# Kernel optimization log

Hardware: AMD Instinct MI355X
Metric: run time of the kernel (lower is better)

Reference implementation:

```python
import jax, jax.numpy as jnp
import numpy as np

B, J, C = 8, 2048, 256
K = 32
H = 8
D = 32  # out_dim per head


def setup_inputs() -> dict:
    key = jax.random.key(0)
    k0, k1, k2, k3, k4, k5 = jax.random.split(key, 6)
    x = jax.random.normal(k0, (B, J, C), dtype=jnp.float32)
    nbr_idx = jax.random.randint(k1, (B, J, K), 0, J)
    s_in = 1.0 / np.sqrt(C)
    s_hd = 1.0 / np.sqrt(H * D)
    Wq = jax.random.uniform(k2, (C, H * D), dtype=jnp.float32, minval=-s_in, maxval=s_in)
    Wk = jax.random.uniform(k3, (C, H * D), dtype=jnp.float32, minval=-s_in, maxval=s_in)
    Wv = jax.random.uniform(k4, (C, H * D), dtype=jnp.float32, minval=-s_in, maxval=s_in)
    Wp = jax.random.uniform(k5, (H * D, D), dtype=jnp.float32, minval=-s_hd, maxval=s_hd)
    return {"x": x, "nbr_idx": nbr_idx, "Wq": Wq, "Wk": Wk, "Wv": Wv, "Wp": Wp}


def reference(x, nbr_idx, Wq, Wk, Wv, Wp):
    b, j, c = x.shape
    q = (x @ Wq).reshape(b, j, H, D)  # [B,J,H,D]
    k = (x @ Wk).reshape(b, j, H, D)
    v = (x @ Wv).reshape(b, j, H, D)
    bidx = jnp.arange(b)[:, None, None]  # [B,1,1]
    k_nbr = k[bidx, nbr_idx]  # [B,J,K,H,D]
    v_nbr = v[bidx, nbr_idx]  # [B,J,K,H,D]
    attn = jnp.einsum("bjhd,bjkhd->bjkh", q, k_nbr) / np.sqrt(D)
    attn = jax.nn.leaky_relu(attn, negative_slope=0.2)
    attn = jax.nn.softmax(attn, axis=2)  # softmax over K neighbors
    out = jnp.einsum("bjkh,bjkhd->bjhd", attn, v_nbr).reshape(b, j, H * D)
    return out @ Wp  # [B,J,D]
```

## Files before the change

### kernel.cpp

```cpp
#include <hip/hip_runtime.h>
#include <hip/hip_bf16.h>


typedef short bf16x8 __attribute__((ext_vector_type(8)));
typedef float f32x4  __attribute__((ext_vector_type(4)));
typedef float f32x2  __attribute__((ext_vector_type(2)));
typedef _Float16 h16x2 __attribute__((ext_vector_type(2)));

__device__ __forceinline__ float bf2f(unsigned short u) {
    union { unsigned int i; float f; } c; c.i = ((unsigned int)u) << 16; return c.f;
}
__device__ __forceinline__ unsigned short f2bf(float f) {
    union { float f; unsigned int i; } c; c.f = f;
    unsigned int r = c.i + 0x7FFFu + ((c.i >> 16) & 1u);
    return (unsigned short)(r >> 16);
}
__device__ __forceinline__ unsigned short f2h(float f) {
    union { _Float16 h; unsigned short u; } c; c.h = (_Float16)f;
    return c.u;
}
__device__ __forceinline__ f32x2 upk(unsigned int u) {
    union { unsigned int i; float f; } lo, hi;
    lo.i = u << 16;
    hi.i = u & 0xffff0000u;
    return (f32x2){lo.f, hi.f};
}

#if defined(__has_builtin)
#if __has_builtin(__builtin_amdgcn_fdot2)
#define HAVE_FDOT2 1
#endif
#endif
__device__ __forceinline__ float dot2acc(unsigned int a, unsigned int b, float acc) {
#ifdef HAVE_FDOT2
    union { unsigned int u; h16x2 v; } ca, cb;
    ca.u = a; cb.u = b;
    return __builtin_amdgcn_fdot2(ca.v, cb.v, acc, false);
#else
    union { unsigned int u; _Float16 h[2]; } ca, cb;
    ca.u = a; cb.u = b;
    return acc + (float)ca.h[0] * (float)cb.h[0] + (float)ca.h[1] * (float)cb.h[1];
#endif
}

__device__ __forceinline__ void gld_lds16(void* lds, const void* g) {
    __builtin_amdgcn_global_load_lds(
        (const __attribute__((address_space(1))) unsigned int*)g,
        (__attribute__((address_space(3))) unsigned int*)lds,
        16, 0, 0);
}

__global__ __launch_bounds__(256) void prep(
    const float* __restrict__ x,
    const float* __restrict__ Wq, const float* __restrict__ Wk,
    const float* __restrict__ Wv, const float* __restrict__ Wp,
    unsigned short* __restrict__ xb, unsigned short* __restrict__ Wt)
{
    const int blk = blockIdx.x, tid = threadIdx.x;
    if (blk < 4096) {
        int t = blk * 256 + tid;
        float4 f = ((const float4*)x)[t];
        ushort4 u;
        u.x = f2bf(f.x); u.y = f2bf(f.y); u.z = f2bf(f.z); u.w = f2bf(f.w);
        ((ushort4*)xb)[t] = u;
        return;
    }
    int wi = blk - 4096;
    int w = wi >> 8, n = wi & 255, t = tid;
    if (w == 0) {
        Wt[(size_t)n * 256 + t] = f2bf(Wq[(size_t)t * 256 + n]);
    } else if (w == 1) {
        Wt[(size_t)(256 + n) * 256 + t] = f2bf(Wk[(size_t)t * 256 + n]);
    } else {
        int h = n >> 5, c = n & 31;
        float acc = 0.f;
#pragma unroll
        for (int d = 0; d < 32; d++)
            acc += Wv[(size_t)t * 256 + h * 32 + d] * Wp[(size_t)(h * 32 + d) * 32 + c];
        Wt[(size_t)(512 + n) * 256 + t] = f2bf(acc);
    }
}

__global__ __launch_bounds__(256) void qkv_mfma(
    const unsigned short* __restrict__ xb,
    const unsigned short* __restrict__ Wt,
    unsigned short* __restrict__ Q, unsigned short* __restrict__ Kp,
    unsigned short* __restrict__ VP)
{
    __shared__ unsigned short Als[128][64];
    __shared__ unsigned short Bls[128][64];

    const unsigned short* Wb = Wt + (size_t)blockIdx.z * 65536;
    unsigned short* Y = (blockIdx.z == 0) ? Q : (blockIdx.z == 1) ? Kp : VP;
    const bool as_f16 = (blockIdx.z != 2);

    const int row0 = blockIdx.x * 128;
    const int col0 = blockIdx.y * 128;
    const int tid  = threadIdx.x;
    const int w    = tid >> 6, l = tid & 63;
    const int wm   = (w >> 1) * 64, wn = (w & 1) * 64;
    const int lm   = l & 15, quad = l >> 4;

    f32x4 acc[4][4];
#pragma unroll
    for (int i = 0; i < 4; i++)
#pragma unroll
        for (int j = 0; j < 4; j++) acc[i][j] = (f32x4){0.f, 0.f, 0.f, 0.f};

    const char* Ab = (const char*)(xb + (size_t)row0 * 256);
    const char* Bb = (const char*)(Wb + (size_t)col0 * 256);

    for (int k0 = 0; k0 < 256; k0 += 64) {
#pragma unroll
        for (int i = 0; i < 4; i++) {
            int s = i * 256 + tid;
            int r = s >> 3, c = s & 7;
            size_t go = (size_t)r * 512 + (size_t)k0 * 2 + c * 16;
            gld_lds16((char*)Als + s * 16, Ab + go);
            gld_lds16((char*)Bls + s * 16, Bb + go);
        }
        __syncthreads();

#pragma unroll
        for (int kk = 0; kk < 64; kk += 32) {
            bf16x8 a[4], b[4];
#pragma unroll
            for (int tm = 0; tm < 4; tm++)
                a[tm] = *(const bf16x8*)&Als[wm + tm * 16 + lm][kk + quad * 8];
#pragma unroll
            for (int tn = 0; tn < 4; tn++)
                b[tn] = *(const bf16x8*)&Bls[wn + tn * 16 + lm][kk + quad * 8];
#pragma unroll
            for (int tm = 0; tm < 4; tm++)
#pragma unroll
                for (int tn = 0; tn < 4; tn++)
                    acc[tm][tn] = __builtin_amdgcn_mfma_f32_16x16x32_bf16(
                        a[tm], b[tn], acc[tm][tn], 0, 0, 0);
        }
        __syncthreads();
    }

#pragma unroll
    for (int tm = 0; tm < 4; tm++) {
        int rbase = row0 + wm + tm * 16 + quad * 4;
#pragma unroll
        for (int tn = 0; tn < 4; tn++) {
            int col = col0 + wn + tn * 16 + lm;
            if (as_f16) {
#pragma unroll
                for (int r = 0; r < 4; r++)
                    Y[(size_t)(rbase + r) * 256 + col] = f2h(acc[tm][tn][r]);
            } else {
#pragma unroll
                for (int r = 0; r < 4; r++)
                    Y[(size_t)(rbase + r) * 256 + col] = f2bf(acc[tm][tn][r]);
            }
        }
    }
}

__global__ __launch_bounds__(256) void attn_wave(
    const unsigned short* __restrict__ qb,
    const unsigned short* __restrict__ kb,
    const unsigned short* __restrict__ vp,
    const int*            __restrict__ nbr,
    float*                __restrict__ out)
{
    const int beta = blockIdx.x;
    const int b    = beta & 7;
    const int jt   = beta >> 3;
    const int tid  = threadIdx.x;
    const int w    = tid >> 6;
    const int l    = tid & 63;
    const int lh   = l & 31;
    const int h5   = l >> 5;
    const int bj   = (b << 11) + jt * 4 + w;
    const size_t bbase = (size_t)b << 19;
    const int* nrow = nbr + (size_t)bj * 32;

    int ko = nrow[lh] << 8;
    int koff[16];
#pragma unroll
    for (int r = 0; r < 16; r++) koff[r] = __shfl(ko, 2 * r + h5);

    uint4 qu = *(const uint4*)(qb + (size_t)bj * 256 + lh * 8);

    uint4 kr[16];
#pragma unroll
    for (int r = 0; r < 16; r++)
        kr[r] = *(const uint4*)(kb + bbase + koff[r] + lh * 8);

    float s[16];
#pragma unroll
    for (int r = 0; r < 16; r++) {
        float a = 0.f;
        a = dot2acc(kr[r].x, qu.x, a);
        a = dot2acc(kr[r].y, qu.y, a);
        a = dot2acc(kr[r].z, qu.z, a);
        a = dot2acc(kr[r].w, qu.w, a);
        a += __shfl_xor(a, 1);
        a += __shfl_xor(a, 2);
        a *= 0.17677669529663687f;
        s[r] = (a > 0.f) ? a : 0.2f * a;
    }

    uint4 vr[16];
#pragma unroll
    for (int r = 0; r < 16; r++)
        vr[r] = *(const uint4*)(vp + bbase + koff[r] + lh * 8);

    float m = s[0];
#pragma unroll
    for (int r = 1; r < 16; r++) m = fmaxf(m, s[r]);
    m = fmaxf(m, __shfl_xor(m, 32));
    float sum = 0.f;
#pragma unroll
    for (int r = 0; r < 16; r++) { s[r] = __expf(s[r] - m); sum += s[r]; }
    sum += __shfl_xor(sum, 32);
    const float inv = 1.0f / sum;
#pragma unroll
    for (int r = 0; r < 16; r++) s[r] *= inv;

    f32x2 a0 = (f32x2){0.f, 0.f}, a1 = a0, a2 = a0, a3 = a0;
#pragma unroll
    for (int r = 0; r < 16; r++) {
        const f32x2 w2 = (f32x2){s[r], s[r]};
        a0 += upk(vr[r].x) * w2;
        a1 += upk(vr[r].y) * w2;
        a2 += upk(vr[r].z) * w2;
        a3 += upk(vr[r].w) * w2;
    }

    float o[8] = {a0.x, a0.y, a1.x, a1.y, a2.x, a2.y, a3.x, a3.y};
#pragma unroll
    for (int i = 0; i < 8; i++) o[i] += __shfl_xor(o[i], 32);
#pragma unroll
    for (int i = 0; i < 8; i++) o[i] += __shfl_xor(o[i], 4);
#pragma unroll
    for (int i = 0; i < 8; i++) o[i] += __shfl_xor(o[i], 8);
#pragma unroll
    for (int i = 0; i < 8; i++) o[i] += __shfl_xor(o[i], 16);

    if (l < 4) {
        float* op = out + (size_t)bj * 32 + l * 8;
        *(float4*)(op)     = make_float4(o[0], o[1], o[2], o[3]);
        *(float4*)(op + 4) = make_float4(o[4], o[5], o[6], o[7]);
    }
}

__global__ __launch_bounds__(256) void fused_all(
    const float* __restrict__ X, const int* __restrict__ nbr,
    const float* __restrict__ Wq, const float* __restrict__ Wk,
    const float* __restrict__ Wv, const float* __restrict__ Wp,
    float* __restrict__ out)
{
    __shared__ float xr[256], qrow[256], xn[256];
    __shared__ float vn[32][256];
    __shared__ int   nb[32];
    __shared__ float sc[32][8], pwv[32][8];
    __shared__ float sp[256], hd[256];
    __shared__ float red[8][32];

    const int bj = blockIdx.x, b = bj >> 11, tid = threadIdx.x;

    xr[tid] = X[(size_t)bj * 256 + tid];
    if (tid < 32) nb[tid] = nbr[(size_t)bj * 32 + tid];
    __syncthreads();

    {
        float acc = 0.f;
#pragma unroll 8
        for (int c = 0; c < 256; c++) acc += xr[c] * Wq[(size_t)c * 256 + tid];
        qrow[tid] = acc;
    }
    __syncthreads();

    for (int i = 0; i < 32; i++) {
        size_t r = (size_t)(b * 2048 + nb[i]);
        xn[tid] = X[r * 256 + tid];
        __syncthreads();
        float ka = 0.f, va = 0.f;
#pragma unroll 8
        for (int c = 0; c < 256; c++) {
            float xc = xn[c];
            ka += xc * Wk[(size_t)c * 256 + tid];
            va += xc * Wv[(size_t)c * 256 + tid];
        }
        vn[i][tid] = va;
        sp[tid] = qrow[tid] * ka;
        __syncthreads();
        if (tid < 8) {
            float s = 0.f;
#pragma unroll
            for (int d = 0; d < 32; d++) s += sp[tid * 32 + d];
            s *= 0.17677669529663687f;
            s = (s > 0.f) ? s : 0.2f * s;
            sc[i][tid] = s;
        }
        __syncthreads();
    }

    {
        const int h = tid & 7, kk = tid >> 3;
        float mx = -1e30f;
#pragma unroll
        for (int i = 0; i < 32; i++) mx = fmaxf(mx, sc[i][h]);
        float ssum = 0.f;
#pragma unroll
        for (int i = 0; i < 32; i++) ssum += __expf(sc[i][h] - mx);
        pwv[kk][h] = __expf(sc[kk][h] - mx) / ssum;
    }
    __syncthreads();

    {
        const int h2 = tid >> 5;
        float acc = 0.f;
#pragma unroll 8
        for (int i = 0; i < 32; i++) acc += pwv[i][h2] * vn[i][tid];
        hd[tid] = acc;
    }
    __syncthreads();

    {
        const int c = tid & 31, ch = tid >> 5;
        float p = 0.f;
#pragma unroll
        for (int i = 0; i < 32; i++) { int r = ch * 32 + i; p += hd[r] * Wp[r * 32 + c]; }
        red[ch][c] = p;
    }
    __syncthreads();

    if (tid < 32) {
        float o = 0.f;
#pragma unroll
        for (int i = 0; i < 8; i++) o += red[i][tid];
        out[(size_t)bj * 32 + tid] = o;
    }
}

extern "C" void kernel_launch(void* const* d_in, const int* in_sizes, int n_in,
                              void* d_out, int out_size, void* d_ws, size_t ws_size,
                              hipStream_t stream) {
    const float* x   = (const float*)d_in[0];
    const int*   nbr = (const int*)d_in[1];
    const float* Wq  = (const float*)d_in[2];
    const float* Wk  = (const float*)d_in[3];
    const float* Wv  = (const float*)d_in[4];
    const float* Wp  = (const float*)d_in[5];
    float*       out = (float*)d_out;

    const size_t ME   = (size_t)16384 * 256;
    const size_t need = (4 * ME + 3 * 65536) * sizeof(unsigned short);

    if (ws_size >= need) {
        unsigned short* q  = (unsigned short*)d_ws;
        unsigned short* k  = q + ME;
        unsigned short* vp = k + ME;
        unsigned short* xb = vp + ME;
        unsigned short* Wt = xb + ME;

        prep<<<4096 + 768, 256, 0, stream>>>(x, Wq, Wk, Wv, Wp, xb, Wt);
        qkv_mfma<<<dim3(128, 2, 3), 256, 0, stream>>>(xb, Wt, q, k, vp);
        attn_wave<<<4096, 256, 0, stream>>>(q, k, vp, nbr, out);
    } else {
        fused_all<<<16384, 256, 0, stream>>>(x, nbr, Wq, Wk, Wv, Wp, out);
    }
}
```

Before: 119.3 us.

## Double-buffer QKV GEMM LDS tiles with XOR swizzle and remapped 1D grid

Restructures the QKV projection GEMM to use a double-buffered LDS pipeline over 32-wide K steps. The next tile's global-to-LDS load is issued while MFMAs run on the current one. It adds an XOR swizzle on the 16-byte chunk index to reduce LDS bank conflicts. It also replaces the 3D grid with a 1D grid remapped so that consecutive blocks spread across XCDs while sharing row tiles. The cost is one barrier per K step instead of two per 64-wide step, plus extra index arithmetic; the overall GEMM is a modest share of the total runtime.

```diff
diff --git a/kernel.cpp b/kernel.cpp
--- a/kernel.cpp
+++ b/kernel.cpp
@@ -87,19 +87,24 @@
     unsigned short* __restrict__ Q, unsigned short* __restrict__ Kp,
     unsigned short* __restrict__ VP)
 {
-    __shared__ unsigned short Als[128][64];
-    __shared__ unsigned short Bls[128][64];
-
-    const unsigned short* Wb = Wt + (size_t)blockIdx.z * 65536;
-    unsigned short* Y = (blockIdx.z == 0) ? Q : (blockIdx.z == 1) ? Kp : VP;
-    const bool as_f16 = (blockIdx.z != 2);
-
-    const int row0 = blockIdx.x * 128;
-    const int col0 = blockIdx.y * 128;
+    __shared__ uint4 AlsV[1024];
+    __shared__ uint4 BlsV[1024];
+
+    const int bid = blockIdx.x;
+    const int wg  = (bid & 7) * 96 + (bid >> 3);
+    const int rt  = wg / 6;
+    const int ct  = wg % 6;
+    const int row0 = rt * 128;
+
+    unsigned short* Y = (ct < 2) ? Q : (ct < 4) ? Kp : VP;
+    const bool as_f16 = (ct < 4);
+    const int  col0   = (ct & 1) * 128;
+
     const int tid  = threadIdx.x;
     const int w    = tid >> 6, l = tid & 63;
     const int wm   = (w >> 1) * 64, wn = (w & 1) * 64;
     const int lm   = l & 15, quad = l >> 4;
+    const int swz  = (lm >> 1) & 3;
 
     f32x4 acc[4][4];
 #pragma unroll
@@ -108,36 +113,50 @@
         for (int j = 0; j < 4; j++) acc[i][j] = (f32x4){0.f, 0.f, 0.f, 0.f};
 
     const char* Ab = (const char*)(xb + (size_t)row0 * 256);
-    const char* Bb = (const char*)(Wb + (size_t)col0 * 256);
-
-    for (int k0 = 0; k0 < 256; k0 += 64) {
-#pragma unroll
-        for (int i = 0; i < 4; i++) {
-            int s = i * 256 + tid;
-            int r = s >> 3, c = s & 7;
-            size_t go = (size_t)r * 512 + (size_t)k0 * 2 + c * 16;
-            gld_lds16((char*)Als + s * 16, Ab + go);
-            gld_lds16((char*)Bls + s * 16, Bb + go);
-        }
+    const char* Bb = (const char*)(Wt + (size_t)(ct * 128) * 256);
+
+    auto stage = [&](int t, int buf) {
+#pragma unroll
+        for (int i = 0; i < 2; i++) {
+            int cid = i * 256 + tid;
+            int r   = cid >> 2;
+            int cs  = cid & 3;
+            int c   = cs ^ ((r >> 1) & 3);
+            size_t go = (size_t)r * 512 + (size_t)t * 64 + (size_t)c * 16;
+            gld_lds16((char*)AlsV + buf * 8192 + cid * 16, Ab + go);
+            gld_lds16((char*)BlsV + buf * 8192 + cid * 16, Bb + go);
+        }
+    };
+
+    stage(0, 0);
+    __syncthreads();
+
+    int cur = 0;
+    for (int t = 0; t < 8; ++t) {
+        if (t < 7) stage(t + 1, cur ^ 1);
+
+        const char* Abase = (const char*)AlsV + cur * 8192;
+        const char* Bbase = (const char*)BlsV + cur * 8192;
+        bf16x8 a[4], b[4];
+#pragma unroll
+        for (int tm = 0; tm < 4; tm++) {
+            int R = wm + tm * 16 + lm;
+            a[tm] = *(const bf16x8*)(Abase + R * 64 + ((quad ^ swz) << 4));
+        }
+#pragma unroll
+        for (int tn = 0; tn < 4; tn++) {
+            int R = wn + tn * 16 + lm;
+            b[tn] = *(const bf16x8*)(Bbase + R * 64 + ((quad ^ swz) << 4));
+        }
+#pragma unroll
+        for (int tm = 0; tm < 4; tm++)
+#pragma unroll
+            for (int tn = 0; tn < 4; tn++)
+                acc[tm][tn] = __builtin_amdgcn_mfma_f32_16x16x32_bf16(
+                    a[tm], b[tn], acc[tm][tn], 0, 0, 0);
+
         __syncthreads();
-
-#pragma unroll
-        for (int kk = 0; kk < 64; kk += 32) {
-            bf16x8 a[4], b[4];
-#pragma unroll
-            for (int tm = 0; tm < 4; tm++)
-                a[tm] = *(const bf16x8*)&Als[wm + tm * 16 + lm][kk + quad * 8];
-#pragma unroll
-            for (int tn = 0; tn < 4; tn++)
-                b[tn] = *(const bf16x8*)&Bls[wn + tn * 16 + lm][kk + quad * 8];
-#pragma unroll
-            for (int tm = 0; tm < 4; tm++)
-#pragma unroll
-                for (int tn = 0; tn < 4; tn++)
-                    acc[tm][tn] = __builtin_amdgcn_mfma_f32_16x16x32_bf16(
-                        a[tm], b[tn], acc[tm][tn], 0, 0, 0);
-        }
-        __syncthreads();
+        cur ^= 1;
     }
 
 #pragma unroll
@@ -360,7 +379,7 @@
         unsigned short* Wt = xb + ME;
 
         prep<<<4096 + 768, 256, 0, stream>>>(x, Wq, Wk, Wv, Wp, xb, Wt);
-        qkv_mfma<<<dim3(128, 2, 3), 256, 0, stream>>>(xb, Wt, q, k, vp);
+        qkv_mfma<<<768, 256, 0, stream>>>(xb, Wt, q, k, vp);
         attn_wave<<<4096, 256, 0, stream>>>(q, k, vp, nbr, out);
     } else {
         fused_all<<<16384, 256, 0, stream>>>(x, nbr, Wq, Wk, Wv, Wp, out);
```

Result: no change. 118.1 us (-1.0%).
